# Optimization experiments

Hardware: AMD Instinct MI355X
Metric: run time of the kernel (lower is better)

The kernel has to match this reference:

```python
import jax, jax.numpy as jnp
import numpy as np

B, T, S = 2, 1024, 2048            # batch, query len, cache size
D, N, KH, H = 4096, 32, 8, 128     # emb_dim, q heads, kv heads, head_dim
ROPE_THETA = 1000000
EPS = 1e-6
K_MASK = jnp.finfo(jnp.bfloat16).min


def _rms_norm(x, scale):
    dtype = x.dtype
    rms = jnp.sqrt(jnp.mean(x.astype(jnp.float32) ** 2, axis=-1, keepdims=True) + EPS)
    return (scale * x / rms).astype(dtype)


def _rope_sincos(positions, head_dim):
    fraction = jnp.arange(0, head_dim, 2, dtype=jnp.float32) / head_dim
    inv_freq = 1.0 / (ROPE_THETA ** fraction)
    sinusoid = jnp.einsum('BT,k->BTk', positions.astype(jnp.float32), inv_freq,
                          precision=jax.lax.Precision.HIGHEST)
    return jnp.sin(sinusoid), jnp.cos(sinusoid)


def _apply_rope(x, sin, cos):
    half = x.shape[-1] // 2
    x1, x2 = x[..., :half], x[..., half:]
    sin, cos = sin[:, :, None, :], cos[:, :, None, :]
    return jnp.concatenate([x1 * cos - x2 * sin, x2 * cos + x1 * sin], axis=-1).astype(x.dtype)


def setup_inputs() -> dict:
    key = jax.random.key(0)
    ks = jax.random.split(key, 8)
    std = 0.01  # nnx.initializers.normal() default stddev
    return {
        'x': jax.random.normal(ks[0], (B, T, D), dtype=jnp.float32),
        'wq': jax.random.normal(ks[1], (D, N, H), dtype=jnp.float32) * std,
        'wk': jax.random.normal(ks[2], (D, KH, H), dtype=jnp.float32) * std,
        'wv': jax.random.normal(ks[3], (D, KH, H), dtype=jnp.float32) * std,
        'wo': jax.random.normal(ks[4], (N, H, D), dtype=jnp.float32) * std,
        'q_scale': jnp.ones((H,), dtype=jnp.float32),
        'k_scale': jnp.ones((H,), dtype=jnp.float32),
        'k_cache': jnp.zeros((B, S, KH, H), dtype=jnp.float32),
        'v_cache': jnp.zeros((B, S, KH, H), dtype=jnp.float32),
        'segment_ids': jnp.ones((B, T), dtype=jnp.int32),
        'num_right_pads': 0,
    }


def reference(x, wq, wk, wv, wo, q_scale, k_scale, k_cache, v_cache, segment_ids, num_right_pads):
    b, t, _ = x.shape
    s = k_cache.shape[1]
    n, kh, h = wq.shape[1], wk.shape[1], wq.shape[2]
    cur_ind = 0  # empty cache (prefill)

    q = _rms_norm(jnp.einsum('BTD,DNH->BTNH', x, wq), q_scale)      # [B,T,N,H]
    key = _rms_norm(jnp.einsum('BSD,DKH->BSKH', x, wk), k_scale)    # [B,T,K,H]
    val = jnp.einsum('BSD,DKH->BSKH', x, wv)                         # [B,T,K,H]

    # start_ind < 0 initially -> count left pads from segment_ids
    start = jnp.sum(jnp.cumsum(segment_ids != 0, axis=-1) == 0, -1).astype(jnp.int32)
    first = jnp.argmax(segment_ids, axis=1)
    pos = jnp.where(segment_ids != 0, jnp.arange(t, dtype=jnp.int32) - first[:, None], 2 ** 30)
    position_ids = pos + cur_ind

    sin, cos = _rope_sincos(position_ids, h)
    q = _apply_rope(q, sin, cos)
    key = _apply_rope(key, sin, cos)

    k_cache = jax.lax.dynamic_update_slice(k_cache, key, (0, cur_ind, 0, 0))
    v_cache = jax.lax.dynamic_update_slice(v_cache, val, (0, cur_ind, 0, 0))

    g = n // kh
    qr = q.reshape(b, t, kh, g, h)
    logits = jnp.einsum('BTHGD,BSHD->BHGTS', qr, k_cache) * (h ** -0.5)

    q_pos = cur_ind + jnp.arange(t, dtype=jnp.int32)[None, :] - start[:, None]
    ts = jnp.arange(s, dtype=jnp.int32)
    kv_seg = ((ts[None, :] >= start[:, None]) & (ts[None, :] < cur_ind + t)).astype(segment_ids.dtype)
    k_pos = ts[None, :] - start[:, None]
    causal = k_pos[:, None, :] <= q_pos[:, :, None]                  # [B,T,S]
    seg_mask = kv_seg[:, None, :] == segment_ids[:, :, None]        # [B,T,S]
    mask = causal & seg_mask

    logits = jnp.where(mask[:, None, None, :, :], logits, K_MASK)
    w = jax.nn.softmax(logits.astype(jnp.float32), axis=-1).astype(logits.dtype)
    qkv = jnp.einsum('BHGTS,BSHD->BTHGD', w, v_cache).reshape(b, t, n, h)
    return jnp.einsum('BTNH,NHD->BTD', qkv, wo)
```

## Files before the change

kernel.cpp:

```cpp
#include <hip/hip_runtime.h>

constexpr int Bc  = 2;
constexpr int Tc  = 1024;
constexpr int Dc  = 4096;
constexpr int NHc = 32;
constexpr int KHc = 8;
constexpr int Hc  = 128;

typedef __bf16 bf16;
typedef bf16  bf16x4  __attribute__((ext_vector_type(4)));
typedef bf16  bf16x8  __attribute__((ext_vector_type(8)));
typedef float floatx4 __attribute__((ext_vector_type(4)));

#define MFMA16(a, b, c) __builtin_amdgcn_mfma_f32_16x16x32_bf16((a), (b), (c), 0, 0, 0)

__device__ __forceinline__ void gload_lds16(const bf16* g, bf16* l) {
    __builtin_amdgcn_global_load_lds(
        (const __attribute__((address_space(1))) void*)g,
        (__attribute__((address_space(3))) void*)l, 16, 0, 0);
}

__global__ void seg_scan(const int* __restrict__ seg, int* __restrict__ start) {
    int b = threadIdx.x;
    if (b >= Bc) return;
    int f = 0;
    for (int t = 0; t < Tc; ++t) {
        if (seg[b * Tc + t] != 0) { f = t; break; }
    }
    start[b] = f;
}

__global__ __launch_bounds__(256) void cvt_f32_bf16(const float* __restrict__ in,
                                                    bf16* __restrict__ out) {
    const size_t i = ((size_t)blockIdx.x * 256 + threadIdx.x) * 8;
    float4 f0 = *(const float4*)(in + i);
    float4 f1 = *(const float4*)(in + i + 4);
    bf16x8 v;
    v[0] = (bf16)f0.x; v[1] = (bf16)f0.y; v[2] = (bf16)f0.z; v[3] = (bf16)f0.w;
    v[4] = (bf16)f1.x; v[5] = (bf16)f1.y; v[6] = (bf16)f1.z; v[7] = (bf16)f1.w;
    *(bf16x8*)(out + i) = v;
}

__global__ __launch_bounds__(256) void transpose_cvt(const float* __restrict__ in,
                                                     bf16* __restrict__ out,
                                                     int R, int C) {
    __shared__ float tile[64][65];
    const int c0 = blockIdx.x * 64, r0 = blockIdx.y * 64;
    const int tx = threadIdx.x & 15, ty = threadIdx.x >> 4;
#pragma unroll
    for (int i = 0; i < 4; ++i) {
        float4 f = *(const float4*)&in[(size_t)(r0 + ty * 4 + i) * C + c0 + tx * 4];
        tile[ty * 4 + i][tx * 4 + 0] = f.x;
        tile[ty * 4 + i][tx * 4 + 1] = f.y;
        tile[ty * 4 + i][tx * 4 + 2] = f.z;
        tile[ty * 4 + i][tx * 4 + 3] = f.w;
    }
    __syncthreads();
#pragma unroll
    for (int i = 0; i < 4; ++i) {
        const int cc = ty * 4 + i;
        bf16x4 v;
        v[0] = (bf16)tile[tx * 4 + 0][cc];
        v[1] = (bf16)tile[tx * 4 + 1][cc];
        v[2] = (bf16)tile[tx * 4 + 2][cc];
        v[3] = (bf16)tile[tx * 4 + 3][cc];
        *(bf16x4*)&out[(size_t)(c0 + cc) * R + r0 + tx * 4] = v;
    }
}

__global__ __launch_bounds__(256) void v_transpose(const bf16* __restrict__ src,
                                                   bf16* __restrict__ dst,
                                                   int srcstride) {
    __shared__ bf16 tl[32][136];
    const int bk = blockIdx.y;
    const int b = bk / KHc, kh = bk % KHc;
    const int t0 = blockIdx.x * 32;
    const int tid = threadIdx.x;
    {
        const int j = tid >> 3;
        const int c = tid & 7;
        const bf16* p = src + (size_t)(b * Tc + t0 + j) * srcstride + kh * Hc + c * 16;
        *(bf16x8*)&tl[j][c * 16]     = *(const bf16x8*)p;
        *(bf16x8*)&tl[j][c * 16 + 8] = *(const bf16x8*)(p + 8);
    }
    __syncthreads();
    {
        const int d = tid >> 1;
        const int toff = (tid & 1) * 16;
        bf16x8 v0, v1;
#pragma unroll
        for (int k = 0; k < 8; ++k) v0[k] = tl[toff + k][d];
#pragma unroll
        for (int k = 0; k < 8; ++k) v1[k] = tl[toff + 8 + k][d];
        bf16* o = dst + ((size_t)bk * Hc + d) * Tc + t0 + toff;
        *(bf16x8*)o       = v0;
        *(bf16x8*)(o + 8) = v1;
    }
}

template <typename OT>
__global__ __launch_bounds__(256) void gemm128(const bf16* __restrict__ A,
                                               const bf16* __restrict__ Bt,
                                               OT* __restrict__ C,
                                               int M, int K, int N) {
    __shared__ alignas(16) bf16 As[128 * 32];
    __shared__ alignas(16) bf16 Bs[128 * 32];
    const int m0 = blockIdx.y * 128, n0 = blockIdx.x * 128;
    const int tid = threadIdx.x;
    const int w = tid >> 6, L = tid & 63, quad = L >> 4, lid = L & 15;
    const int wm = (w & 1) * 64, wn = (w >> 1) * 64;

    const int srow = w * 32 + (L >> 2);
    const int chk  = (L & 3) ^ ((L >> 3) & 3);
    const bf16* gA = A  + (size_t)(m0 + srow) * K + chk * 8;
    const bf16* gB = Bt + (size_t)(n0 + srow) * K + chk * 8;
    bf16* lA0 = &As[(w * 32) * 32];
    bf16* lA1 = &As[(w * 32 + 16) * 32];
    bf16* lB0 = &Bs[(w * 32) * 32];
    bf16* lB1 = &Bs[(w * 32 + 16) * 32];

    const bf16* ap[4]; const bf16* bp[4];
#pragma unroll
    for (int i = 0; i < 4; ++i) {
        const int ra = wm + i * 16 + lid;
        ap[i] = &As[ra * 32 + (quad ^ ((ra >> 1) & 3)) * 8];
        const int rb = wn + i * 16 + lid;
        bp[i] = &Bs[rb * 32 + (quad ^ ((rb >> 1) & 3)) * 8];
    }

    floatx4 acc[4][4] = {};

    for (int k0 = 0; k0 < K; k0 += 32) {
        __syncthreads();
        gload_lds16(gA + k0,                  lA0);
        gload_lds16(gA + (size_t)16 * K + k0, lA1);
        gload_lds16(gB + k0,                  lB0);
        gload_lds16(gB + (size_t)16 * K + k0, lB1);
        __syncthreads();

        bf16x8 af[4], bfr[4];
#pragma unroll
        for (int i = 0; i < 4; ++i) af[i]  = *(const bf16x8*)ap[i];
#pragma unroll
        for (int j = 0; j < 4; ++j) bfr[j] = *(const bf16x8*)bp[j];
#pragma unroll
        for (int i = 0; i < 4; ++i)
#pragma unroll
            for (int j = 0; j < 4; ++j)
                acc[i][j] = MFMA16(af[i], bfr[j], acc[i][j]);
    }

#pragma unroll
    for (int i = 0; i < 4; ++i) {
#pragma unroll
        for (int r = 0; r < 4; ++r) {
            const size_t row = (size_t)(m0 + wm + i * 16 + quad * 4 + r);
#pragma unroll
            for (int j = 0; j < 4; ++j)
                C[row * N + (n0 + wn + j * 16 + lid)] = (OT)acc[i][j][r];
        }
    }
}

template <typename OT>
__global__ __launch_bounds__(256, 2) void gemm_ring192(const bf16* __restrict__ A,
                                                       const bf16* __restrict__ Bt,
                                                       OT* __restrict__ C,
                                                       int M, int K, int N) {
    __shared__ alignas(16) bf16 ring[3][10240];
    const int m0 = blockIdx.y * 128, n0 = blockIdx.x * 192;
    const int tid = threadIdx.x;
    const int w = tid >> 6, L = tid & 63, quad = L >> 4, lid = L & 15;
    const int wr = w >> 1, wc = w & 1;

    const int srow = tid >> 2;
    const int schk = ((tid & 3) ^ ((tid >> 3) & 3)) * 8;
    const bf16* gA = A  + (size_t)(m0 + srow) * K + schk;
    const bf16* gB = Bt + (size_t)(n0 + srow) * K + schk;
    const size_t K64 = (size_t)64 * K, K128 = (size_t)128 * K;
    const int ldsA0 = (w * 16) * 32;
    const int ldsA1 = (64 + w * 16) * 32;
    const int ldsB0 = 4096 + (w * 16) * 32;
    const int ldsB1 = 4096 + (64 + w * 16) * 32;
    const int ldsB2 = 4096 + (128 + w * 16) * 32;

    int offA[4], offB[6];
#pragma unroll
    for (int m = 0; m < 4; ++m) {
        const int row = wr * 64 + m * 16 + lid;
        offA[m] = row * 32 + ((quad ^ ((row >> 1) & 3)) * 8);
    }
#pragma unroll
    for (int n = 0; n < 6; ++n) {
        const int row = wc * 96 + n * 16 + lid;
        offB[n] = 4096 + row * 32 + ((quad ^ ((row >> 1) & 3)) * 8);
    }

    const int NT = K >> 5;

    auto stage = [&](int kt, int sl) {
        bf16* sb = ring[sl];
        const size_t ko = (size_t)kt << 5;
        gload_lds16(gA + ko,         sb + ldsA0);
        gload_lds16(gA + K64 + ko,   sb + ldsA1);
        gload_lds16(gB + ko,         sb + ldsB0);
        gload_lds16(gB + K64 + ko,   sb + ldsB1);
        gload_lds16(gB + K128 + ko,  sb + ldsB2);
    };

    stage(0, 0); stage(1, 1);
    asm volatile("s_waitcnt vmcnt(5)" ::: "memory");
    __builtin_amdgcn_s_barrier();
    __builtin_amdgcn_sched_barrier(0);

    floatx4 acc[4][6] = {};
    int cur = 0;

    for (int t = 0; t < NT; ++t) {
        int ts = t + 2; if (ts >= NT) ts -= NT;
        int ss = cur + 2; if (ss >= 3) ss -= 3;
        stage(ts, ss);

        const bf16* sb = ring[cur];
        bf16x8 af[4], bfr[6];
#pragma unroll
        for (int m = 0; m < 4; ++m) af[m]  = *(const bf16x8*)(sb + offA[m]);
#pragma unroll
        for (int n = 0; n < 6; ++n) bfr[n] = *(const bf16x8*)(sb + offB[n]);

        __builtin_amdgcn_s_setprio(1);
#pragma unroll
        for (int m = 0; m < 4; ++m)
#pragma unroll
            for (int n = 0; n < 6; ++n)
                acc[m][n] = MFMA16(af[m], bfr[n], acc[m][n]);
        __builtin_amdgcn_s_setprio(0);

        asm volatile("s_waitcnt vmcnt(5)" ::: "memory");
        __builtin_amdgcn_s_barrier();
        __builtin_amdgcn_sched_barrier(0);
        cur = (cur == 2) ? 0 : cur + 1;
    }

    asm volatile("s_waitcnt vmcnt(0)" ::: "memory");

#pragma unroll
    for (int m = 0; m < 4; ++m) {
#pragma unroll
        for (int r = 0; r < 4; ++r) {
            const size_t row = (size_t)(m0 + wr * 64 + m * 16 + quad * 4 + r);
#pragma unroll
            for (int n = 0; n < 6; ++n)
                C[row * N + (n0 + wc * 96 + n * 16 + lid)] = (OT)acc[m][n][r];
        }
    }
}

__global__ __launch_bounds__(256) void rms_rope(bf16* __restrict__ buf,
                                                const float* __restrict__ scale,
                                                const int* __restrict__ start,
                                                int nheads, int rowstride) {
    const int gid = blockIdx.x * 4 + (threadIdx.x >> 6);
    const int L   = threadIdx.x & 63;
    const int h   = gid % nheads;
    const int t   = (gid / nheads) % Tc;
    const int b   = gid / (nheads * Tc);
    bf16* p = buf + (size_t)(b * Tc + t) * rowstride + h * Hc;

    float x1 = (float)p[L], x2 = (float)p[L + 64];
    float ss = x1 * x1 + x2 * x2;
#pragma unroll
    for (int off = 1; off < 64; off <<= 1) ss += __shfl_xor(ss, off);
    const float inv = 1.f / sqrtf(ss * (1.0f / 128.0f) + 1e-6f);
    const float y1 = scale[L] * x1 * inv;
    const float y2 = scale[L + 64] * x2 * inv;

    const int   pos = t - start[b];
    const float fr  = (float)L * (1.0f / 64.0f);
    const float invf = exp2f(-19.9315686f * fr);
    const float ang = (float)pos * invf;
    float sn, cs;
    sincosf(ang, &sn, &cs);

    p[L]      = (bf16)(y1 * cs - y2 * sn);
    p[L + 64] = (bf16)(y2 * cs + y1 * sn);
}

__global__ __launch_bounds__(256) void attn_kernel(const bf16* __restrict__ q,
                                                   const bf16* __restrict__ k,
                                                   const bf16* __restrict__ vt,
                                                   bf16* __restrict__ outp,
                                                   const int* __restrict__ start,
                                                   int qstride, int kstride) {
    __shared__ alignas(16) bf16 Ks[32 * 128];
    __shared__ alignas(16) bf16 VT[128 * 32];
    __shared__ alignas(16) bf16 pS[4][16][40];

    const int tblk = blockIdx.x, n = blockIdx.y, b = blockIdx.z;
    const int kh   = n >> 2;
    const int tid  = threadIdx.x, w = tid >> 6, L = tid & 63;
    const int quad = L >> 4, lid = L & 15;
    const int t0   = tblk * 64 + w * 16;
    const int st   = start[b];

    const bf16* qrow = q + (size_t)(b * Tc + t0 + lid) * qstride + n * Hc;
    bf16x8 aqf[4];
#pragma unroll
    for (int c = 0; c < 4; ++c) aqf[c] = *(const bf16x8*)(qrow + c * 32 + quad * 8);

    const int kr0 = w * 8 + (L >> 4);
    const int kr1 = kr0 + 4;
    const bf16* gK0 = k + (size_t)(b * Tc + kr0) * kstride + kh * Hc
                        + (((L & 15) ^ (kr0 & 15)) * 8);
    const bf16* gK1 = k + (size_t)(b * Tc + kr1) * kstride + kh * Hc
                        + (((L & 15) ^ (kr1 & 15)) * 8);
    bf16* lK0 = &Ks[(w * 8) * 128];
    bf16* lK1 = &Ks[(w * 8 + 4) * 128];

    const int vd0 = (w * 2) * 16 + (L >> 2);
    const int vd1 = vd0 + 16;
    const bf16* vbase = vt + (size_t)((b * KHc + kh) * Hc) * Tc;
    const bf16* gV0 = vbase + (size_t)vd0 * Tc + (((L & 3) ^ (vd0 & 3) ^ ((vd0 >> 2) & 3)) * 8);
    const bf16* gV1 = vbase + (size_t)vd1 * Tc + (((L & 3) ^ (vd1 & 3) ^ ((vd1 >> 2) & 3)) * 8);
    bf16* lV0 = &VT[(w * 2) * 512];
    bf16* lV1 = &VT[(w * 2 + 1) * 512];

    const bf16* kf[4][2];
#pragma unroll
    for (int c = 0; c < 4; ++c) {
        kf[c][0] = &Ks[lid * 128        + (((c * 4 + quad) ^ lid) * 8)];
        kf[c][1] = &Ks[(16 + lid) * 128 + (((c * 4 + quad) ^ lid) * 8)];
    }
    const int vpos = (quad ^ (lid & 3) ^ ((lid >> 2) & 3)) * 8;
    const bf16* vf[8];
#pragma unroll
    for (int cg = 0; cg < 8; ++cg) vf[cg] = &VT[(cg * 16 + lid) * 32 + vpos];

    floatx4 oacc[8] = {};
    float lsum[4] = {0.f, 0.f, 0.f, 0.f};
    const int sEnd = tblk * 64 + 64;

    for (int s0 = 0; s0 < sEnd; s0 += 32) {
        __syncthreads();
        gload_lds16(gK0 + (size_t)s0 * kstride, lK0);
        gload_lds16(gK1 + (size_t)s0 * kstride, lK1);
        gload_lds16(gV0 + s0, lV0);
        gload_lds16(gV1 + s0, lV1);
        __syncthreads();

        floatx4 sc0 = {0.f, 0.f, 0.f, 0.f}, sc1 = {0.f, 0.f, 0.f, 0.f};
#pragma unroll
        for (int c = 0; c < 4; ++c) {
            sc0 = MFMA16(aqf[c], *(const bf16x8*)kf[c][0], sc0);
            sc1 = MFMA16(aqf[c], *(const bf16x8*)kf[c][1], sc1);
        }

#pragma unroll
        for (int r = 0; r < 4; ++r) {
            const int tq  = t0 + quad * 4 + r;
            const int sk0 = s0 + lid, sk1 = s0 + 16 + lid;
            const float p0 = (sk0 <= tq && sk0 >= st)
                               ? __expf(sc0[r] * 0.08838834764831845f - 16.f) : 0.f;
            const float p1 = (sk1 <= tq && sk1 >= st)
                               ? __expf(sc1[r] * 0.08838834764831845f - 16.f) : 0.f;
            lsum[r] += p0 + p1;
            pS[w][quad * 4 + r][lid]      = (bf16)p0;
            pS[w][quad * 4 + r][16 + lid] = (bf16)p1;
        }
        asm volatile("s_waitcnt lgkmcnt(0)" ::: "memory");

        bf16x8 pa = *(const bf16x8*)&pS[w][lid][quad * 8];
#pragma unroll
        for (int cg = 0; cg < 8; ++cg)
            oacc[cg] = MFMA16(pa, *(const bf16x8*)vf[cg], oacc[cg]);
    }

#pragma unroll
    for (int r = 0; r < 4; ++r) {
        lsum[r] += __shfl_xor(lsum[r], 1);
        lsum[r] += __shfl_xor(lsum[r], 2);
        lsum[r] += __shfl_xor(lsum[r], 4);
        lsum[r] += __shfl_xor(lsum[r], 8);
    }

#pragma unroll
    for (int cg = 0; cg < 8; ++cg) {
#pragma unroll
        for (int r = 0; r < 4; ++r) {
            const int t = t0 + quad * 4 + r;
            outp[((size_t)(b * Tc + t) * NHc + n) * Hc + cg * 16 + lid] =
                (bf16)(oacc[cg][r] / lsum[r]);
        }
    }
}

extern "C" void kernel_launch(void* const* d_in, const int* in_sizes, int n_in,
                              void* d_out, int out_size, void* d_ws, size_t ws_size,
                              hipStream_t stream) {
    const float* x       = (const float*)d_in[0];
    const float* wq      = (const float*)d_in[1];
    const float* wk      = (const float*)d_in[2];
    const float* wv      = (const float*)d_in[3];
    const float* wo      = (const float*)d_in[4];
    const float* q_scale = (const float*)d_in[5];
    const float* k_scale = (const float*)d_in[6];
    const int*   seg     = (const int*)d_in[9];
    float*       out     = (float*)d_out;

    char* ws = (char*)d_ws;
    bf16* wcomb = (bf16*)(ws);
    bf16* vtb   = (bf16*)(ws + (32ull << 20));
    bf16* qkvb  = (bf16*)(ws + (48ull << 20));
    bf16* xb    = (bf16*)(ws + (72ull << 20));
    bf16* ab    = xb;
    int*  stb   = (int*) (ws + (88ull << 20));

    seg_scan<<<1, 64, 0, stream>>>(seg, stb);

    cvt_f32_bf16<<<(Bc * Tc * Dc) / (256 * 8), 256, 0, stream>>>(x, xb);

    transpose_cvt<<<dim3(64, 64), 256, 0, stream>>>(wq, wcomb, Dc, NHc * Hc);
    transpose_cvt<<<dim3(16, 64), 256, 0, stream>>>(wk, wcomb + (size_t)4096 * Dc, Dc, KHc * Hc);
    transpose_cvt<<<dim3(16, 64), 256, 0, stream>>>(wv, wcomb + (size_t)5120 * Dc, Dc, KHc * Hc);

    gemm_ring192<bf16><<<dim3(32, 16), 256, 0, stream>>>(xb, wcomb, qkvb,
                                                         Bc * Tc, Dc, 6144);

    rms_rope<<<(Bc * Tc * NHc) / 4, 256, 0, stream>>>(qkvb, q_scale, stb, NHc, 6144);
    rms_rope<<<(Bc * Tc * KHc) / 4, 256, 0, stream>>>(qkvb + 4096, k_scale, stb, KHc, 6144);

    v_transpose<<<dim3(Tc / 32, Bc * KHc), 256, 0, stream>>>(qkvb + 5120, vtb, 6144);

    transpose_cvt<<<dim3(64, 64), 256, 0, stream>>>(wo, wcomb, NHc * Hc, Dc);

    attn_kernel<<<dim3(Tc / 64, NHc, Bc), 256, 0, stream>>>(
        qkvb, qkvb + 4096, vtb, ab, stb, 6144, 6144);

    gemm128<float><<<dim3(32, 16), 256, 0, stream>>>(ab, wcomb, out,
                                                     Bc * Tc, NHc * Hc, Dc);
}
```

Measured before the change: 520.7 us.

## Pipeline output projection GEMM with triple-buffered LDS ring and async prefetch

Swaps the single-buffered output projection GEMM for a 3-slot LDS ring that prefetches tiles two K-steps ahead using direct global-to-LDS loads. Each iteration then needs one barrier with a partial vmcnt wait instead of two full syncs, and MFMA priority is raised with setprio. This aims to hide global load latency behind the matrix math, at the cost of more LDS per block (48KB). Near the end the ring wraps and issues redundant loads of early tiles, which waste some bandwidth but leave the results unchanged.

Result: faster. 499.3 us (-4.1%).

```diff
diff --git a/kernel.cpp b/kernel.cpp
--- a/kernel.cpp
+++ b/kernel.cpp
@@ -99,65 +99,93 @@
 }
 
 template <typename OT>
-__global__ __launch_bounds__(256) void gemm128(const bf16* __restrict__ A,
-                                               const bf16* __restrict__ Bt,
-                                               OT* __restrict__ C,
-                                               int M, int K, int N) {
-    __shared__ alignas(16) bf16 As[128 * 32];
-    __shared__ alignas(16) bf16 Bs[128 * 32];
+__global__ __launch_bounds__(256, 2) void gemm_ring128(const bf16* __restrict__ A,
+                                                       const bf16* __restrict__ Bt,
+                                                       OT* __restrict__ C,
+                                                       int M, int K, int N) {
+    __shared__ alignas(16) bf16 ring[3][8192];
     const int m0 = blockIdx.y * 128, n0 = blockIdx.x * 128;
     const int tid = threadIdx.x;
     const int w = tid >> 6, L = tid & 63, quad = L >> 4, lid = L & 15;
-    const int wm = (w & 1) * 64, wn = (w >> 1) * 64;
-
-    const int srow = w * 32 + (L >> 2);
-    const int chk  = (L & 3) ^ ((L >> 3) & 3);
-    const bf16* gA = A  + (size_t)(m0 + srow) * K + chk * 8;
-    const bf16* gB = Bt + (size_t)(n0 + srow) * K + chk * 8;
-    bf16* lA0 = &As[(w * 32) * 32];
-    bf16* lA1 = &As[(w * 32 + 16) * 32];
-    bf16* lB0 = &Bs[(w * 32) * 32];
-    bf16* lB1 = &Bs[(w * 32 + 16) * 32];
-
-    const bf16* ap[4]; const bf16* bp[4];
-#pragma unroll
-    for (int i = 0; i < 4; ++i) {
-        const int ra = wm + i * 16 + lid;
-        ap[i] = &As[ra * 32 + (quad ^ ((ra >> 1) & 3)) * 8];
-        const int rb = wn + i * 16 + lid;
-        bp[i] = &Bs[rb * 32 + (quad ^ ((rb >> 1) & 3)) * 8];
-    }
+    const int wr = w >> 1, wc = w & 1;
+
+    const int srow = tid >> 2;
+    const int schk = ((tid & 3) ^ ((tid >> 3) & 3)) * 8;
+    const bf16* gA = A  + (size_t)(m0 + srow) * K + schk;
+    const bf16* gB = Bt + (size_t)(n0 + srow) * K + schk;
+    const size_t K64 = (size_t)64 * K;
+    const int ldsA0 = (w * 16) * 32;
+    const int ldsA1 = (64 + w * 16) * 32;
+    const int ldsB0 = 4096 + (w * 16) * 32;
+    const int ldsB1 = 4096 + (64 + w * 16) * 32;
+
+    int offA[4], offB[4];
+#pragma unroll
+    for (int m = 0; m < 4; ++m) {
+        const int row = wr * 64 + m * 16 + lid;
+        offA[m] = row * 32 + ((quad ^ ((row >> 1) & 3)) * 8);
+    }
+#pragma unroll
+    for (int n = 0; n < 4; ++n) {
+        const int row = wc * 64 + n * 16 + lid;
+        offB[n] = 4096 + row * 32 + ((quad ^ ((row >> 1) & 3)) * 8);
+    }
+
+    const int NT = K >> 5;
+
+    auto stage = [&](int kt, int sl) {
+        bf16* sb = ring[sl];
+        const size_t ko = (size_t)kt << 5;
+        gload_lds16(gA + ko,       sb + ldsA0);
+        gload_lds16(gA + K64 + ko, sb + ldsA1);
+        gload_lds16(gB + ko,       sb + ldsB0);
+        gload_lds16(gB + K64 + ko, sb + ldsB1);
+    };
+
+    stage(0, 0); stage(1, 1);
+    asm volatile("s_waitcnt vmcnt(4)" ::: "memory");
+    __builtin_amdgcn_s_barrier();
+    __builtin_amdgcn_sched_barrier(0);
 
     floatx4 acc[4][4] = {};
-
-    for (int k0 = 0; k0 < K; k0 += 32) {
-        __syncthreads();
-        gload_lds16(gA + k0,                  lA0);
-        gload_lds16(gA + (size_t)16 * K + k0, lA1);
-        gload_lds16(gB + k0,                  lB0);
-        gload_lds16(gB + (size_t)16 * K + k0, lB1);
-        __syncthreads();
-
+    int cur = 0;
+
+    for (int t = 0; t < NT; ++t) {
+        int ts = t + 2; if (ts >= NT) ts -= NT;
+        int ss = cur + 2; if (ss >= 3) ss -= 3;
+        stage(ts, ss);
+
+        const bf16* sb = ring[cur];
         bf16x8 af[4], bfr[4];
 #pragma unroll
-        for (int i = 0; i < 4; ++i) af[i]  = *(const bf16x8*)ap[i];
-#pragma unroll
-        for (int j = 0; j < 4; ++j) bfr[j] = *(const bf16x8*)bp[j];
-#pragma unroll
-        for (int i = 0; i < 4; ++i)
-#pragma unroll
-            for (int j = 0; j < 4; ++j)
-                acc[i][j] = MFMA16(af[i], bfr[j], acc[i][j]);
-    }
-
-#pragma unroll
-    for (int i = 0; i < 4; ++i) {
+        for (int m = 0; m < 4; ++m) af[m]  = *(const bf16x8*)(sb + offA[m]);
+#pragma unroll
+        for (int n = 0; n < 4; ++n) bfr[n] = *(const bf16x8*)(sb + offB[n]);
+
+        __builtin_amdgcn_s_setprio(1);
+#pragma unroll
+        for (int m = 0; m < 4; ++m)
+#pragma unroll
+            for (int n = 0; n < 4; ++n)
+                acc[m][n] = MFMA16(af[m], bfr[n], acc[m][n]);
+        __builtin_amdgcn_s_setprio(0);
+
+        asm volatile("s_waitcnt vmcnt(4)" ::: "memory");
+        __builtin_amdgcn_s_barrier();
+        __builtin_amdgcn_sched_barrier(0);
+        cur = (cur == 2) ? 0 : cur + 1;
+    }
+
+    asm volatile("s_waitcnt vmcnt(0)" ::: "memory");
+
+#pragma unroll
+    for (int m = 0; m < 4; ++m) {
 #pragma unroll
         for (int r = 0; r < 4; ++r) {
-            const size_t row = (size_t)(m0 + wm + i * 16 + quad * 4 + r);
-#pragma unroll
-            for (int j = 0; j < 4; ++j)
-                C[row * N + (n0 + wn + j * 16 + lid)] = (OT)acc[i][j][r];
+            const size_t row = (size_t)(m0 + wr * 64 + m * 16 + quad * 4 + r);
+#pragma unroll
+            for (int n = 0; n < 4; ++n)
+                C[row * N + (n0 + wc * 64 + n * 16 + lid)] = (OT)acc[m][n][r];
         }
     }
 }
@@ -436,6 +464,6 @@
     attn_kernel<<<dim3(Tc / 64, NHc, Bc), 256, 0, stream>>>(
         qkvb, qkvb + 4096, vtb, ab, stb, 6144, 6144);
 
-    gemm128<float><<<dim3(32, 16), 256, 0, stream>>>(ab, wcomb, out,
-                                                     Bc * Tc, NHc * Hc, Dc);
-}
+    gemm_ring128<float><<<dim3(32, 16), 256, 0, stream>>>(ab, wcomb, out,
+                                                          Bc * Tc, NHc * Hc, Dc);
+}
```
